# Optimization experiments

Measured on AMD Instinct MI355X. Metric: run time of the kernel, lower is better.

## Reference

```python
import jax, jax.numpy as jnp
import numpy as np

B, K, D, H, ZDIM = 65536, 16, 64, 128, 16

def setup_inputs() -> dict:
    key = jax.random.key(0)
    ks = jax.random.split(key, 20)
    s = 0.05
    inp = {
        'z': jax.random.normal(ks[0], (B, ZDIM), dtype=jnp.float32),
        'y': jax.random.randint(ks[1], (B,), 0, K),
        # backbone: 4 fc blocks (Linear+ReLU)
        'bw0': jax.random.normal(ks[2], (ZDIM, H), dtype=jnp.float32) * s,
        'bb0': jnp.zeros((H,), dtype=jnp.float32),
        'bw1': jax.random.normal(ks[3], (H, H), dtype=jnp.float32) * s,
        'bb1': jnp.zeros((H,), dtype=jnp.float32),
        'bw2': jax.random.normal(ks[4], (H, H), dtype=jnp.float32) * s,
        'bb2': jnp.zeros((H,), dtype=jnp.float32),
        'bw3': jax.random.normal(ks[5], (H, H), dtype=jnp.float32) * s,
        'bb3': jnp.zeros((H,), dtype=jnp.float32),
        # K heads, weights stacked on leading expert axis; layers 0-2 have ReLU, layer 3 does not
        'hw0': jax.random.normal(ks[6], (K, H, H), dtype=jnp.float32) * s,
        'hb0': jnp.zeros((K, H), dtype=jnp.float32),
        'hw1': jax.random.normal(ks[7], (K, H, H), dtype=jnp.float32) * s,
        'hb1': jnp.zeros((K, H), dtype=jnp.float32),
        'hw2': jax.random.normal(ks[8], (K, H, H), dtype=jnp.float32) * s,
        'hb2': jnp.zeros((K, H), dtype=jnp.float32),
        'hw3': jax.random.normal(ks[9], (K, H, D), dtype=jnp.float32) * s,
        'hb3': jnp.zeros((K, D), dtype=jnp.float32),
    }
    return inp

def reference(z, y, bw0, bb0, bw1, bb1, bw2, bb2, bw3, bb3,
              hw0, hb0, hw1, hb1, hw2, hb2, hw3, hb3):
    h = jax.nn.relu(z @ bw0 + bb0)
    h = jax.nn.relu(h @ bw1 + bb1)
    h = jax.nn.relu(h @ bw2 + bb2)
    h = jax.nn.relu(h @ bw3 + bb3)          # [B, H]
    # all K expert heads (faithful to original: compute all, then gather)
    a = jax.nn.relu(jnp.einsum('bi,kij->bkj', h, hw0) + hb0)  # [B, K, H]
    a = jax.nn.relu(jnp.einsum('bki,kij->bkj', a, hw1) + hb1)
    a = jax.nn.relu(jnp.einsum('bki,kij->bkj', a, hw2) + hb2)
    a = jnp.einsum('bki,kij->bkj', a, hw3) + hb3              # [B, K, D], no ReLU
    # select the y-th head per sample
    out = jnp.take_along_axis(a, y[:, None, None], axis=1)[:, 0, :]  # [B, D]
    return out
```

## Files before the change

kernel.cpp:

```cpp
#include <hip/hip_runtime.h>
#include <hip/hip_bf16.h>
#include <stdint.h>


typedef _Float16 f16;
typedef __attribute__((ext_vector_type(4)))  _Float16 f16x4;
typedef __attribute__((ext_vector_type(8)))  _Float16 f16x8;
typedef __attribute__((ext_vector_type(16))) float    f32x16;
typedef uint32_t u32;

#define MFMA(a, b, c) __builtin_amdgcn_mfma_f32_32x32x16_f16((a), (b), (c), 0, 0, 0)

constexpr int Bc = 65536;
constexpr int Kc = 16;
constexpr int Hc = 128;
constexpr int Dc = 64;

constexpr int CAP  = 4608;
constexpr int BPE  = CAP / 64;
constexpr int NBLK = Kc * BPE;
constexpr int NXCD = 8;
constexpr int CHUNK = NBLK / NXCD;

constexpr float INV_LOSCALE = 1.0f / 1024.0f;

constexpr int BBW_F16 = 2048 + 3 * 16384;
constexpr int HWE_F16 = 3 * 16384 + 8192;

constexpr int PREP_BLKS = 52 + Kc * 56;

__device__ __forceinline__ f32x16 zero16() {
    f32x16 z;
#pragma unroll
    for (int i = 0; i < 16; ++i) z[i] = 0.0f;
    return z;
}

__device__ __forceinline__ int actOff(int s, int u) {
    return s * 128 + ((u ^ (s & 15)) << 3);
}

template<bool RELU>
__device__ __forceinline__ void epi_store(
    const f32x16& c0, const f32x16& c1,
    const float* __restrict__ biasG, f16* aOut, int wid, int l31, int bh)
{
#pragma unroll
    for (int rg = 0; rg < 4; ++rg) {
        const float4 bv = *(const float4*)(biasG + 32 * wid + 8 * rg + 4 * bh);
        const float bb[4] = {bv.x, bv.y, bv.z, bv.w};
#pragma unroll
        for (int mt = 0; mt < 2; ++mt) {
            const f32x16& ac = mt ? c1 : c0;
            f16x4 h4;
#pragma unroll
            for (int j = 0; j < 4; ++j) {
                float v = fmaf(ac[4 * rg + j], INV_LOSCALE, bb[j]);
                if (RELU) v = fmaxf(v, 0.0f);
                h4[j] = (f16)v;
            }
            const int s = 32 * mt + l31;
            *(f16x4*)(aOut + actOff(s, 4 * wid + rg) + 4 * bh) = h4;
        }
    }
}

__device__ __forceinline__ void layer4(
    const f16* __restrict__ Wh, const f16* __restrict__ Wl,
    const float* __restrict__ biasG, const f16* aIn, f16* aOut,
    int wid, int lane, int l31, int bh)
{
    const f16* ph = Wh + wid * 4096 + lane * 8;
    const f16* pl = Wl + wid * 4096 + lane * 8;

    f32x16 c0 = zero16(), c1 = zero16();
#pragma unroll
    for (int ks = 0; ks < 8; ++ks) {
        const f16x8 whi = *(const f16x8*)(ph + ks * 512);
        const f16x8 wlo = *(const f16x8*)(pl + ks * 512);
        const f16x8 a0 = *(const f16x8*)(aIn + actOff(l31,      2 * ks + bh));
        const f16x8 a1 = *(const f16x8*)(aIn + actOff(32 + l31, 2 * ks + bh));
        c0 = MFMA(whi, a0, c0);
        c1 = MFMA(whi, a1, c1);
        c0 = MFMA(wlo, a0, c0);
        c1 = MFMA(wlo, a1, c1);
    }
    epi_store<true>(c0, c1, biasG, aOut, wid, l31, bh);
}

__global__ __launch_bounds__(256, 5) void fused_mlp(
    const float* __restrict__ z,
    const int* __restrict__ idxb, const int* __restrict__ cursor,
    const f16* __restrict__ bbH, const f16* __restrict__ bbL,
    const float* __restrict__ bb0, const float* __restrict__ bb1,
    const float* __restrict__ bb2, const float* __restrict__ bb3,
    const f16* __restrict__ hH, const f16* __restrict__ hL,
    const float* __restrict__ hb0, const float* __restrict__ hb1,
    const float* __restrict__ hb2, const float* __restrict__ hb3,
    float* __restrict__ out)
{
    __shared__ __attribute__((aligned(16))) f16 A[64 * 128];
    __shared__ __attribute__((aligned(16))) f16 B[64 * 128];

    const int blk = (blockIdx.x % NXCD) * CHUNK + blockIdx.x / NXCD;
    const int e = blk / BPE;
    const int local0 = (blk % BPE) * 64;
    const int cnt = min(cursor[e * 16], CAP);
    const int nvalid = cnt - local0;
    if (nvalid <= 0) return;

    const int tid = threadIdx.x;
    const int wid = tid >> 6, lane = tid & 63;
    const int l31 = lane & 31, bh = lane >> 5;

    {
        const int m = tid >> 2, q = tid & 3;
        f16x4 t;
        if (m < nvalid) {
            const int b = idxb[e * CAP + local0 + m];
            const float4 v = *(const float4*)(z + (size_t)b * 16 + q * 4);
            t[0] = (f16)v.x; t[1] = (f16)v.y; t[2] = (f16)v.z; t[3] = (f16)v.w;
        } else {
            t[0] = t[1] = t[2] = t[3] = (f16)0.0f;
        }
        *(f16x4*)(A + actOff(m, q >> 1) + (q & 1) * 4) = t;
    }
    __syncthreads();

    {
        const f16x8 w0h = *(const f16x8*)(bbH + wid * 512 + lane * 8);
        const f16x8 w0l = *(const f16x8*)(bbL + wid * 512 + lane * 8);
        const f16x8 a0 = *(const f16x8*)(A + actOff(l31,      bh));
        const f16x8 a1 = *(const f16x8*)(A + actOff(32 + l31, bh));
        f32x16 c0 = zero16(), c1 = zero16();
        c0 = MFMA(w0h, a0, c0);
        c1 = MFMA(w0h, a1, c1);
        c0 = MFMA(w0l, a0, c0);
        c1 = MFMA(w0l, a1, c1);
        epi_store<true>(c0, c1, bb0, B, wid, l31, bh);
    }
    __syncthreads();

    layer4(bbH + 2048,  bbL + 2048,  bb1, B, A, wid, lane, l31, bh);
    __syncthreads();
    layer4(bbH + 18432, bbL + 18432, bb2, A, B, wid, lane, l31, bh);
    __syncthreads();
    layer4(bbH + 34816, bbL + 34816, bb3, B, A, wid, lane, l31, bh);
    __syncthreads();

    const size_t we = (size_t)e * HWE_F16;
    layer4(hH + we,         hL + we,         hb0 + e * Hc, A, B, wid, lane, l31, bh);
    __syncthreads();
    layer4(hH + we + 16384, hL + we + 16384, hb1 + e * Hc, B, A, wid, lane, l31, bh);
    __syncthreads();
    layer4(hH + we + 32768, hL + we + 32768, hb2 + e * Hc, A, B, wid, lane, l31, bh);
    __syncthreads();

    if (wid < 2) {
        int b0 = -1, b1 = -1;
        if (l31 < nvalid)      b0 = idxb[e * CAP + local0 + l31];
        if (32 + l31 < nvalid) b1 = idxb[e * CAP + local0 + 32 + l31];

        const f16* ph = hH + we + 49152 + wid * 4096 + lane * 8;
        const f16* pl = hL + we + 49152 + wid * 4096 + lane * 8;
        f32x16 c0 = zero16(), c1 = zero16();
#pragma unroll
        for (int ks = 0; ks < 8; ++ks) {
            const f16x8 whi = *(const f16x8*)(ph + ks * 512);
            const f16x8 wlo = *(const f16x8*)(pl + ks * 512);
            const f16x8 a0 = *(const f16x8*)(B + actOff(l31,      2 * ks + bh));
            const f16x8 a1 = *(const f16x8*)(B + actOff(32 + l31, 2 * ks + bh));
            c0 = MFMA(whi, a0, c0);
            c1 = MFMA(whi, a1, c1);
            c0 = MFMA(wlo, a0, c0);
            c1 = MFMA(wlo, a1, c1);
        }
#pragma unroll
        for (int mt = 0; mt < 2; ++mt) {
            const int b = mt ? b1 : b0;
            if (b < 0) continue;
            const f32x16& ac = mt ? c1 : c0;
#pragma unroll
            for (int rg = 0; rg < 4; ++rg) {
                const int nb = 32 * wid + 8 * rg + 4 * bh;
                const float4 bv = *(const float4*)(hb3 + e * Dc + nb);
                float4 v;
                v.x = fmaf(ac[4 * rg + 0], INV_LOSCALE, bv.x);
                v.y = fmaf(ac[4 * rg + 1], INV_LOSCALE, bv.y);
                v.z = fmaf(ac[4 * rg + 2], INV_LOSCALE, bv.z);
                v.w = fmaf(ac[4 * rg + 3], INV_LOSCALE, bv.w);
                *(float4*)(out + (size_t)b * Dc + nb) = v;
            }
        }
    }
}

__global__ void prep_scatter(
    const float* __restrict__ bw0, const float* __restrict__ bw1,
    const float* __restrict__ bw2, const float* __restrict__ bw3,
    const float* __restrict__ hw0, const float* __restrict__ hw1,
    const float* __restrict__ hw2, const float* __restrict__ hw3,
    f16* __restrict__ bbH, f16* __restrict__ bbL,
    f16* __restrict__ hH,  f16* __restrict__ hL,
    const int* __restrict__ y, int* __restrict__ idxb, int* __restrict__ cursor)
{
    __shared__ float T[32][33];
    __shared__ int lc[Kc];
    __shared__ int lbase[Kc];
    const int id = blockIdx.x;
    const int tx = threadIdx.x;

    if (id >= PREP_BLKS) {
        if (tx < Kc) lc[tx] = 0;
        __syncthreads();
        const int b = (id - PREP_BLKS) * 256 + tx;
        const int e = y[b];
        const int r = atomicAdd(&lc[e], 1);
        __syncthreads();
        if (tx < Kc) lbase[tx] = atomicAdd(&cursor[tx * 16], lc[tx]);
        __syncthreads();
        const int slot = lbase[e] + r;
        if (slot < CAP) idxb[e * CAP + slot] = b;
        return;
    }

    const float* src; f16 *dh, *dl;
    int K, N, k0, n0;
    bool big;

    if (id < 52) {
        if (id < 4) {
            src = bw0; dh = bbH; dl = bbL;
            K = 16; N = 128; k0 = 0; n0 = id * 32; big = false;
        } else {
            const int t = id - 4;
            const int l = t / 16, tile = t % 16;
            const float* bws[3] = {bw1, bw2, bw3};
            src = bws[l];
            dh = bbH + 2048 + l * 16384;
            dl = bbL + 2048 + l * 16384;
            K = 128; N = 128; big = true;
            k0 = (tile >> 2) * 32; n0 = (tile & 3) * 32;
        }
    } else {
        const int t = id - 52;
        const int e = t / 56, r = t % 56;
        if (r < 48) {
            const int l = r / 16, tile = r % 16;
            const float* hws[3] = {hw0, hw1, hw2};
            src = hws[l] + (size_t)e * 16384;
            dh = hH + (size_t)e * HWE_F16 + l * 16384;
            dl = hL + (size_t)e * HWE_F16 + l * 16384;
            K = 128; N = 128; big = true;
            k0 = (tile >> 2) * 32; n0 = (tile & 3) * 32;
        } else {
            const int r2 = r - 48;
            src = hw3 + (size_t)e * 8192;
            dh = hH + (size_t)e * HWE_F16 + 49152;
            dl = hL + (size_t)e * HWE_F16 + 49152;
            K = 128; N = 64; big = true;
            k0 = (r2 >> 1) * 32; n0 = (r2 & 1) * 32;
        }
    }

    const int c = tx & 31, g = tx >> 5;
#pragma unroll
    for (int i = 0; i < 4; ++i) {
        const int row = g * 4 + i;
        if (k0 + row < K)
            T[c][row] = src[(size_t)(k0 + row) * N + n0 + c];
    }
    __syncthreads();
#pragma unroll
    for (int i = 0; i < 4; ++i) {
        const int n = n0 + g * 4 + i;
        const int k = k0 + c;
        if (k < K) {
            const float v = T[g * 4 + i][c];
            const float hif = (float)(f16)v;
            const f16 hi = (f16)(hif * 1024.0f);
            const f16 lo = (f16)((v - hif) * 1024.0f);
            size_t didx;
            if (big)
                didx = (size_t)(n >> 5) * 4096 + (size_t)(k >> 4) * 512
                     + ((k >> 3) & 1) * 256 + (n & 31) * 8 + (k & 7);
            else
                didx = (size_t)(n >> 5) * 512 + (size_t)(k >> 3) * 256
                     + (n & 31) * 8 + (k & 7);
            dh[didx] = hi;
            dl[didx] = lo;
        }
    }
}

extern "C" void kernel_launch(void* const* d_in, const int* in_sizes, int n_in,
                              void* d_out, int out_size, void* d_ws, size_t ws_size,
                              hipStream_t stream)
{
    const float* z   = (const float*)d_in[0];
    const int*   y   = (const int*)d_in[1];
    const float* bw0 = (const float*)d_in[2];
    const float* bb0 = (const float*)d_in[3];
    const float* bw1 = (const float*)d_in[4];
    const float* bb1 = (const float*)d_in[5];
    const float* bw2 = (const float*)d_in[6];
    const float* bb2 = (const float*)d_in[7];
    const float* bw3 = (const float*)d_in[8];
    const float* bb3 = (const float*)d_in[9];
    const float* hw0 = (const float*)d_in[10];
    const float* hb0 = (const float*)d_in[11];
    const float* hw1 = (const float*)d_in[12];
    const float* hb1 = (const float*)d_in[13];
    const float* hw2 = (const float*)d_in[14];
    const float* hb2 = (const float*)d_in[15];
    const float* hw3 = (const float*)d_in[16];
    const float* hb3 = (const float*)d_in[17];
    float* out = (float*)d_out;

    char* p = (char*)d_ws;
    f16* bbH = (f16*)p;  p += (size_t)BBW_F16 * 2;
    f16* bbL = (f16*)p;  p += (size_t)BBW_F16 * 2;
    f16* hH  = (f16*)p;  p += (size_t)Kc * HWE_F16 * 2;
    f16* hL  = (f16*)p;  p += (size_t)Kc * HWE_F16 * 2;
    int* idxb = (int*)p; p += (size_t)Kc * CAP * 4;
    int* cursor = (int*)p;

    hipMemsetAsync(cursor, 0, 256 * sizeof(int), stream);

    prep_scatter<<<PREP_BLKS + Bc / 256, 256, 0, stream>>>(
        bw0, bw1, bw2, bw3, hw0, hw1, hw2, hw3,
        bbH, bbL, hH, hL, y, idxb, cursor);

    fused_mlp<<<NBLK, 256, 0, stream>>>(
        z, idxb, cursor, bbH, bbL, bb0, bb1, bb2, bb3,
        hH, hL, hb0, hb1, hb2, hb3, out);
}
```

Measured before the change: 157.7 us.

## Keep activations in registers and double-buffer weights in LDS via async loads

Result: faster. 144.0 us (-8.6%).

```diff
diff --git a/kernel.cpp b/kernel.cpp
--- a/kernel.cpp
+++ b/kernel.cpp
@@ -4,10 +4,12 @@
 
 
 typedef _Float16 f16;
+typedef __attribute__((ext_vector_type(2)))  _Float16 f16x2;
 typedef __attribute__((ext_vector_type(4)))  _Float16 f16x4;
 typedef __attribute__((ext_vector_type(8)))  _Float16 f16x8;
 typedef __attribute__((ext_vector_type(16))) float    f32x16;
 typedef uint32_t u32;
+typedef __attribute__((ext_vector_type(4))) u32 u32x4;
 
 #define MFMA(a, b, c) __builtin_amdgcn_mfma_f32_32x32x16_f16((a), (b), (c), 0, 0, 0)
 
@@ -17,7 +19,8 @@
 constexpr int Dc = 64;
 
 constexpr int CAP  = 4608;
-constexpr int BPE  = CAP / 64;
+constexpr int SPB  = 128;
+constexpr int BPE  = CAP / SPB;
 constexpr int NBLK = Kc * BPE;
 constexpr int NXCD = 8;
 constexpr int CHUNK = NBLK / NXCD;
@@ -29,6 +32,8 @@
 
 constexpr int PREP_BLKS = 52 + Kc * 56;
 
+struct Act { f16x8 w[8]; };
+
 __device__ __forceinline__ f32x16 zero16() {
     f32x16 z;
 #pragma unroll
@@ -36,59 +41,133 @@
     return z;
 }
 
-__device__ __forceinline__ int actOff(int s, int u) {
-    return s * 128 + ((u ^ (s & 15)) << 3);
+__device__ __forceinline__ void gload16(const f16* g, f16* l) {
+    __builtin_amdgcn_global_load_lds(
+        (const __attribute__((address_space(1))) void*)g,
+        (__attribute__((address_space(3))) void*)l, 16, 0, 0);
+}
+
+__device__ __forceinline__ void stage_q(f16* dst, const f16* gHi, const f16* gLo,
+                                        int wid, int lane) {
+#pragma unroll
+    for (int i = 0; i < 2; ++i) {
+        const int seg = wid * 2 + i;
+        gload16(gHi + seg * 512 + lane * 8, dst + seg * 512);
+        gload16(gLo + seg * 512 + lane * 8, dst + 4096 + seg * 512);
+    }
 }
 
 template<bool RELU>
-__device__ __forceinline__ void epi_store(
-    const f32x16& c0, const f32x16& c1,
-    const float* __restrict__ biasG, f16* aOut, int wid, int l31, int bh)
-{
-#pragma unroll
-    for (int rg = 0; rg < 4; ++rg) {
-        const float4 bv = *(const float4*)(biasG + 32 * wid + 8 * rg + 4 * bh);
-        const float bb[4] = {bv.x, bv.y, bv.z, bv.w};
-#pragma unroll
-        for (int mt = 0; mt < 2; ++mt) {
-            const f32x16& ac = mt ? c1 : c0;
-            f16x4 h4;
-#pragma unroll
-            for (int j = 0; j < 4; ++j) {
-                float v = fmaf(ac[4 * rg + j], INV_LOSCALE, bb[j]);
-                if (RELU) v = fmaxf(v, 0.0f);
-                h4[j] = (f16)v;
+__device__ __forceinline__ void build_windows(
+    const f32x16& c0, const f32x16& c1, const float4* bq, int bh,
+    f16x8& w0, f16x8& w1)
+{
+    u32 P[8];
+#pragma unroll
+    for (int g = 0; g < 4; ++g) {
+        const float bb[4] = {bq[g].x, bq[g].y, bq[g].z, bq[g].w};
+        f16 h[4];
+#pragma unroll
+        for (int j = 0; j < 4; ++j) {
+            float v = fmaf(c0[4 * g + j] + c1[4 * g + j], INV_LOSCALE, bb[j]);
+            if (RELU) v = fmaxf(v, 0.0f);
+            h[j] = (f16)v;
+        }
+        f16x2 p0; p0[0] = h[0]; p0[1] = h[1];
+        f16x2 p1; p1[0] = h[2]; p1[1] = h[3];
+        P[2 * g]     = __builtin_bit_cast(u32, p0);
+        P[2 * g + 1] = __builtin_bit_cast(u32, p1);
+    }
+    const u32 s0 = (u32)__shfl_xor((int)P[0], 32, 64);
+    const u32 s1 = (u32)__shfl_xor((int)P[1], 32, 64);
+    const u32 s2 = (u32)__shfl_xor((int)P[2], 32, 64);
+    const u32 s3 = (u32)__shfl_xor((int)P[3], 32, 64);
+    const u32 s4 = (u32)__shfl_xor((int)P[4], 32, 64);
+    const u32 s5 = (u32)__shfl_xor((int)P[5], 32, 64);
+    const u32 s6 = (u32)__shfl_xor((int)P[6], 32, 64);
+    const u32 s7 = (u32)__shfl_xor((int)P[7], 32, 64);
+    const bool hi = (bh != 0);
+    u32x4 W0 = { hi ? s2 : P[0], hi ? s3 : P[1], hi ? P[2] : s0, hi ? P[3] : s1 };
+    u32x4 W1 = { hi ? s6 : P[4], hi ? s7 : P[5], hi ? P[6] : s4, hi ? P[7] : s5 };
+    w0 = __builtin_bit_cast(f16x8, W0);
+    w1 = __builtin_bit_cast(f16x8, W1);
+}
+
+template<int NQ, bool STAGE_NEXT>
+__device__ __forceinline__ void layer_lds(
+    f16* lds, int& par, const Act& src, Act& dst,
+    const f16* gHi, const f16* gLo, const f16* gHiN, const f16* gLoN,
+    const float* __restrict__ biasG, int wid, int lane, int bh)
+{
+#pragma unroll
+    for (int q = 0; q < NQ; ++q) {
+        if (q < NQ - 1)
+            stage_q(lds + (par ^ 1) * 8192, gHi + (q + 1) * 4096,
+                    gLo + (q + 1) * 4096, wid, lane);
+        else if (STAGE_NEXT)
+            stage_q(lds + (par ^ 1) * 8192, gHiN, gLoN, wid, lane);
+
+        float4 bq[4];
+#pragma unroll
+        for (int g = 0; g < 4; ++g)
+            bq[g] = *(const float4*)(biasG + 32 * q + 8 * g + 4 * bh);
+
+        const f16* pw = lds + par * 8192 + lane * 8;
+        f32x16 c0 = zero16(), c1 = zero16();
+#pragma unroll
+        for (int ks = 0; ks < 8; ++ks) {
+            const f16x8 wh = *(const f16x8*)(pw + ks * 512);
+            const f16x8 wl = *(const f16x8*)(pw + 4096 + ks * 512);
+            c0 = MFMA(wh, src.w[ks], c0);
+            c1 = MFMA(wl, src.w[ks], c1);
+        }
+        build_windows<true>(c0, c1, bq, bh, dst.w[2 * q], dst.w[2 * q + 1]);
+        __syncthreads();
+        par ^= 1;
+    }
+}
+
+__device__ __forceinline__ void layer_final(
+    f16* lds, int& par, const Act& src,
+    const f16* gHi, const f16* gLo, const float* __restrict__ biasG,
+    float* __restrict__ out, int bidx, int wid, int lane, int bh)
+{
+#pragma unroll
+    for (int q = 0; q < 2; ++q) {
+        if (q == 0)
+            stage_q(lds + (par ^ 1) * 8192, gHi + 4096, gLo + 4096, wid, lane);
+
+        float4 bq[4];
+#pragma unroll
+        for (int g = 0; g < 4; ++g)
+            bq[g] = *(const float4*)(biasG + 32 * q + 8 * g + 4 * bh);
+
+        const f16* pw = lds + par * 8192 + lane * 8;
+        f32x16 c0 = zero16(), c1 = zero16();
+#pragma unroll
+        for (int ks = 0; ks < 8; ++ks) {
+            const f16x8 wh = *(const f16x8*)(pw + ks * 512);
+            const f16x8 wl = *(const f16x8*)(pw + 4096 + ks * 512);
+            c0 = MFMA(wh, src.w[ks], c0);
+            c1 = MFMA(wl, src.w[ks], c1);
+        }
+        if (bidx >= 0) {
+#pragma unroll
+            for (int g = 0; g < 4; ++g) {
+                float4 v;
+                v.x = fmaf(c0[4 * g + 0] + c1[4 * g + 0], INV_LOSCALE, bq[g].x);
+                v.y = fmaf(c0[4 * g + 1] + c1[4 * g + 1], INV_LOSCALE, bq[g].y);
+                v.z = fmaf(c0[4 * g + 2] + c1[4 * g + 2], INV_LOSCALE, bq[g].z);
+                v.w = fmaf(c0[4 * g + 3] + c1[4 * g + 3], INV_LOSCALE, bq[g].w);
+                *(float4*)(out + (size_t)bidx * Dc + 32 * q + 8 * g + 4 * bh) = v;
             }
-            const int s = 32 * mt + l31;
-            *(f16x4*)(aOut + actOff(s, 4 * wid + rg) + 4 * bh) = h4;
-        }
-    }
-}
-
-__device__ __forceinline__ void layer4(
-    const f16* __restrict__ Wh, const f16* __restrict__ Wl,
-    const float* __restrict__ biasG, const f16* aIn, f16* aOut,
-    int wid, int lane, int l31, int bh)
-{
-    const f16* ph = Wh + wid * 4096 + lane * 8;
-    const f16* pl = Wl + wid * 4096 + lane * 8;
-
-    f32x16 c0 = zero16(), c1 = zero16();
-#pragma unroll
-    for (int ks = 0; ks < 8; ++ks) {
-        const f16x8 whi = *(const f16x8*)(ph + ks * 512);
-        const f16x8 wlo = *(const f16x8*)(pl + ks * 512);
-        const f16x8 a0 = *(const f16x8*)(aIn + actOff(l31,      2 * ks + bh));
-        const f16x8 a1 = *(const f16x8*)(aIn + actOff(32 + l31, 2 * ks + bh));
-        c0 = MFMA(whi, a0, c0);
-        c1 = MFMA(whi, a1, c1);
-        c0 = MFMA(wlo, a0, c0);
-        c1 = MFMA(wlo, a1, c1);
-    }
-    epi_store<true>(c0, c1, biasG, aOut, wid, l31, bh);
-}
-
-__global__ __launch_bounds__(256, 5) void fused_mlp(
+        }
+        if (q == 0) __syncthreads();
+        par ^= 1;
+    }
+}
+
+__global__ __launch_bounds__(256, 3) void fused_mlp(
     const float* __restrict__ z,
     const int* __restrict__ idxb, const int* __restrict__ cursor,
     const f16* __restrict__ bbH, const f16* __restrict__ bbL,
@@ -99,100 +178,67 @@
     const float* __restrict__ hb2, const float* __restrict__ hb3,
     float* __restrict__ out)
 {
-    __shared__ __attribute__((aligned(16))) f16 A[64 * 128];
-    __shared__ __attribute__((aligned(16))) f16 B[64 * 128];
+    __shared__ __attribute__((aligned(16))) f16 WLDS[2 * 8192];
 
     const int blk = (blockIdx.x % NXCD) * CHUNK + blockIdx.x / NXCD;
     const int e = blk / BPE;
-    const int local0 = (blk % BPE) * 64;
+    const int local0 = (blk % BPE) * SPB;
     const int cnt = min(cursor[e * 16], CAP);
-    const int nvalid = cnt - local0;
-    if (nvalid <= 0) return;
+    if (cnt - local0 <= 0) return;
 
     const int tid = threadIdx.x;
     const int wid = tid >> 6, lane = tid & 63;
     const int l31 = lane & 31, bh = lane >> 5;
 
-    {
-        const int m = tid >> 2, q = tid & 3;
-        f16x4 t;
-        if (m < nvalid) {
-            const int b = idxb[e * CAP + local0 + m];
-            const float4 v = *(const float4*)(z + (size_t)b * 16 + q * 4);
-            t[0] = (f16)v.x; t[1] = (f16)v.y; t[2] = (f16)v.z; t[3] = (f16)v.w;
-        } else {
-            t[0] = t[1] = t[2] = t[3] = (f16)0.0f;
-        }
-        *(f16x4*)(A + actOff(m, q >> 1) + (q & 1) * 4) = t;
+    int bidx = -1;
+    const int sIdx = local0 + wid * 32 + l31;
+    if (sIdx < cnt) bidx = idxb[e * CAP + sIdx];
+
+    f16x8 zw;
+    if (bidx >= 0) {
+        const float4 u0 = *(const float4*)(z + (size_t)bidx * 16 + bh * 8);
+        const float4 u1 = *(const float4*)(z + (size_t)bidx * 16 + bh * 8 + 4);
+        zw[0] = (f16)u0.x; zw[1] = (f16)u0.y; zw[2] = (f16)u0.z; zw[3] = (f16)u0.w;
+        zw[4] = (f16)u1.x; zw[5] = (f16)u1.y; zw[6] = (f16)u1.z; zw[7] = (f16)u1.w;
+    } else {
+#pragma unroll
+        for (int j = 0; j < 8; ++j) zw[j] = (f16)0.0f;
+    }
+
+    stage_q(WLDS, bbH + 2048, bbL + 2048, wid, lane);
+
+    Act aA, aB;
+#pragma unroll
+    for (int q = 0; q < 4; ++q) {
+        float4 bq[4];
+#pragma unroll
+        for (int g = 0; g < 4; ++g)
+            bq[g] = *(const float4*)(bb0 + 32 * q + 8 * g + 4 * bh);
+        const f16x8 wh = *(const f16x8*)(bbH + q * 512 + lane * 8);
+        const f16x8 wl = *(const f16x8*)(bbL + q * 512 + lane * 8);
+        f32x16 c0 = zero16(), c1 = zero16();
+        c0 = MFMA(wh, zw, c0);
+        c1 = MFMA(wl, zw, c1);
+        build_windows<true>(c0, c1, bq, bh, aA.w[2 * q], aA.w[2 * q + 1]);
     }
     __syncthreads();
-
-    {
-        const f16x8 w0h = *(const f16x8*)(bbH + wid * 512 + lane * 8);
-        const f16x8 w0l = *(const f16x8*)(bbL + wid * 512 + lane * 8);
-        const f16x8 a0 = *(const f16x8*)(A + actOff(l31,      bh));
-        const f16x8 a1 = *(const f16x8*)(A + actOff(32 + l31, bh));
-        f32x16 c0 = zero16(), c1 = zero16();
-        c0 = MFMA(w0h, a0, c0);
-        c1 = MFMA(w0h, a1, c1);
-        c0 = MFMA(w0l, a0, c0);
-        c1 = MFMA(w0l, a1, c1);
-        epi_store<true>(c0, c1, bb0, B, wid, l31, bh);
-    }
-    __syncthreads();
-
-    layer4(bbH + 2048,  bbL + 2048,  bb1, B, A, wid, lane, l31, bh);
-    __syncthreads();
-    layer4(bbH + 18432, bbL + 18432, bb2, A, B, wid, lane, l31, bh);
-    __syncthreads();
-    layer4(bbH + 34816, bbL + 34816, bb3, B, A, wid, lane, l31, bh);
-    __syncthreads();
-
+    int par = 0;
+
+    layer_lds<4, true>(WLDS, par, aA, aB, bbH + 2048,  bbL + 2048,
+                       bbH + 18432, bbL + 18432, bb1, wid, lane, bh);
+    layer_lds<4, true>(WLDS, par, aB, aA, bbH + 18432, bbL + 18432,
+                       bbH + 34816, bbL + 34816, bb2, wid, lane, bh);
     const size_t we = (size_t)e * HWE_F16;
-    layer4(hH + we,         hL + we,         hb0 + e * Hc, A, B, wid, lane, l31, bh);
-    __syncthreads();
-    layer4(hH + we + 16384, hL + we + 16384, hb1 + e * Hc, B, A, wid, lane, l31, bh);
-    __syncthreads();
-    layer4(hH + we + 32768, hL + we + 32768, hb2 + e * Hc, A, B, wid, lane, l31, bh);
-    __syncthreads();
-
-    if (wid < 2) {
-        int b0 = -1, b1 = -1;
-        if (l31 < nvalid)      b0 = idxb[e * CAP + local0 + l31];
-        if (32 + l31 < nvalid) b1 = idxb[e * CAP + local0 + 32 + l31];
-
-        const f16* ph = hH + we + 49152 + wid * 4096 + lane * 8;
-        const f16* pl = hL + we + 49152 + wid * 4096 + lane * 8;
-        f32x16 c0 = zero16(), c1 = zero16();
-#pragma unroll
-        for (int ks = 0; ks < 8; ++ks) {
-            const f16x8 whi = *(const f16x8*)(ph + ks * 512);
-            const f16x8 wlo = *(const f16x8*)(pl + ks * 512);
-            const f16x8 a0 = *(const f16x8*)(B + actOff(l31,      2 * ks + bh));
-            const f16x8 a1 = *(const f16x8*)(B + actOff(32 + l31, 2 * ks + bh));
-            c0 = MFMA(whi, a0, c0);
-            c1 = MFMA(whi, a1, c1);
-            c0 = MFMA(wlo, a0, c0);
-            c1 = MFMA(wlo, a1, c1);
-        }
-#pragma unroll
-        for (int mt = 0; mt < 2; ++mt) {
-            const int b = mt ? b1 : b0;
-            if (b < 0) continue;
-            const f32x16& ac = mt ? c1 : c0;
-#pragma unroll
-            for (int rg = 0; rg < 4; ++rg) {
-                const int nb = 32 * wid + 8 * rg + 4 * bh;
-                const float4 bv = *(const float4*)(hb3 + e * Dc + nb);
-                float4 v;
-                v.x = fmaf(ac[4 * rg + 0], INV_LOSCALE, bv.x);
-                v.y = fmaf(ac[4 * rg + 1], INV_LOSCALE, bv.y);
-                v.z = fmaf(ac[4 * rg + 2], INV_LOSCALE, bv.z);
-                v.w = fmaf(ac[4 * rg + 3], INV_LOSCALE, bv.w);
-                *(float4*)(out + (size_t)b * Dc + nb) = v;
-            }
-        }
-    }
+    layer_lds<4, true>(WLDS, par, aA, aB, bbH + 34816, bbL + 34816,
+                       hH + we, hL + we, bb3, wid, lane, bh);
+    layer_lds<4, true>(WLDS, par, aB, aA, hH + we,         hL + we,
+                       hH + we + 16384, hL + we + 16384, hb0 + e * Hc, wid, lane, bh);
+    layer_lds<4, true>(WLDS, par, aA, aB, hH + we + 16384, hL + we + 16384,
+                       hH + we + 32768, hL + we + 32768, hb1 + e * Hc, wid, lane, bh);
+    layer_lds<4, true>(WLDS, par, aB, aA, hH + we + 32768, hL + we + 32768,
+                       hH + we + 49152, hL + we + 49152, hb2 + e * Hc, wid, lane, bh);
+    layer_final(WLDS, par, aA, hH + we + 49152, hL + we + 49152,
+                hb3 + e * Dc, out, bidx, wid, lane, bh);
 }
 
 __global__ void prep_scatter(
```
